# Performance work log

Hardware: AMD Instinct MI355X
Metric: run time of the kernel (lower is better)

Reference implementation:

```python
import jax, jax.numpy as jnp
import numpy as np
import math

DIM = 384
NH = 8
HR = 4.0
LOGIT_MAX = math.log(1.0 / 0.01)
EPS_LN = 1e-5
EPS_NORM = 1e-12


def setup_inputs() -> dict:
    key = jax.random.key(0)
    ks = jax.random.split(key, 6)
    B, C, H, W = 16, DIM, 64, 64
    hid = int(DIM * HR)
    s = lambda k, shape: (jax.random.normal(k, shape, jnp.float32) * 0.02)
    return {
        "x": jax.random.normal(ks[0], (B, C, H, W), jnp.float32),
        "g1": jnp.ones((C,), jnp.float32),
        "beta1": jnp.zeros((C,), jnp.float32),
        "w_qkv": s(ks[1], (3 * C, C)),
        "b_qkv": jnp.zeros((3 * C,), jnp.float32),
        "logit_scale": jnp.log(10.0) * jnp.ones((NH, 1, 1), jnp.float32),
        "w_proj": s(ks[2], (C, C)),
        "b_proj": jnp.zeros((C,), jnp.float32),
        "g2": jnp.ones((C,), jnp.float32),
        "beta2": jnp.zeros((C,), jnp.float32),
        "w_ffn1": s(ks[3], (hid, C)),
        "b_ffn1": jnp.zeros((hid,), jnp.float32),
        "w_ffn2": s(ks[4], (C, hid)),
        "b_ffn2": jnp.zeros((C,), jnp.float32),
    }


def _ln_channels(x, g, b):
    # LayerNorm over channel axis of NCHW (ReshapeLayerNorm equivalent)
    m = x.mean(axis=1, keepdims=True)
    v = x.var(axis=1, keepdims=True)
    return (x - m) / jnp.sqrt(v + EPS_LN) * g[None, :, None, None] + b[None, :, None, None]


def _conv1x1(x, w, b):
    # 1x1 conv == per-pixel matmul: w [O,C], x [B,C,H,W]
    return jnp.einsum('oc,bchw->bohw', w, x) + b[None, :, None, None]


def reference(x, g1, beta1, w_qkv, b_qkv, logit_scale, w_proj, b_proj,
              g2, beta2, w_ffn1, b_ffn1, w_ffn2, b_ffn2):
    B, C, H, W = x.shape
    ch = C // NH  # per-head channel dim

    # --- channel self-attention branch ---
    xn = _ln_channels(x, g1, beta1)
    qkv = _conv1x1(xn, w_qkv, b_qkv)                 # [B, 3C, H, W]
    qkv = qkv.reshape(B, NH, 3 * ch, H * W)          # [B, L, 3c, N]
    q, k, v = jnp.split(qkv, 3, axis=2)              # each [B, L, c, N]

    qn = q / jnp.maximum(jnp.linalg.norm(q, axis=-1, keepdims=True), EPS_NORM)
    kn = k / jnp.maximum(jnp.linalg.norm(k, axis=-1, keepdims=True), EPS_NORM)
    scale = jnp.exp(jnp.minimum(logit_scale, LOGIT_MAX))  # [L,1,1]

    attn = jnp.einsum('blcn,bldn->blcd', qn, kn) * scale[None]  # [B, L, c, c]
    attn = jax.nn.softmax(attn, axis=-1)
    out = jnp.einsum('blcd,bldn->blcn', attn, v)     # [B, L, c, N]
    out = out.reshape(B, C, H, W)
    out = _conv1x1(out, w_proj, b_proj)
    x = x + out

    # --- FFN branch ---
    yn = _ln_channels(x, g2, beta2)
    h = jax.nn.gelu(_conv1x1(yn, w_ffn1, b_ffn1), approximate=False)
    ff = _conv1x1(h, w_ffn2, b_ffn2)
    return x + ff
```

## Files before the change

kernel.cpp:

```cpp
#include <hip/hip_runtime.h>
#include <hip/hip_bf16.h>

#define DIM 384
#define NH 8
#define CH 48
#define NPIX 4096
#define LOGIT_MAX 4.6051701859880914f

typedef unsigned int uint;
typedef __attribute__((ext_vector_type(4))) float f32x4;
typedef __attribute__((ext_vector_type(8))) short bf16x8;

union f2u { float f; uint u; };
__device__ __forceinline__ float bf_lo(uint u) { f2u t; t.u = u << 16; return t.f; }
__device__ __forceinline__ float bf_hi(uint u) { f2u t; t.u = u & 0xffff0000u; return t.f; }
__device__ __forceinline__ unsigned short bfbits(float f) {
  __hip_bfloat16 h = __float2bfloat16(f);
  return *reinterpret_cast<unsigned short*>(&h);
}

__device__ __forceinline__ void gload16(const void* g, void* l) {
  using gp = const __attribute__((address_space(1))) uint*;
  using lp = __attribute__((address_space(3))) uint*;
  __builtin_amdgcn_global_load_lds((gp)(unsigned long long)g,
                                   (lp)(uint)(unsigned long long)l, 16, 0, 0);
}

#define LNP 390
__global__ __launch_bounds__(256) void ln_t_kernel(const float* __restrict__ x,
                                                   const float* __restrict__ g,
                                                   const float* __restrict__ be,
                                                   __hip_bfloat16* __restrict__ out) {
  __shared__ __hip_bfloat16 T[64 * LNP];
  __shared__ float ps1[4][64], ps2[4][64], mArr[64], iArr[64];
  int b = blockIdx.y, n0 = blockIdx.x * 64;
  int nl = threadIdx.x & 63, cg = threadIdx.x >> 6;
  const float* xb = x + ((size_t)b * DIM) * NPIX + n0 + nl;
  float s1 = 0.f, s2 = 0.f;
#pragma unroll 4
  for (int i = 0; i < 96; ++i) {
    int c = cg * 96 + i;
    float v = xb[(size_t)c * NPIX];
    s1 += v; s2 += v * v;
    T[nl * LNP + c] = __float2bfloat16(v);
  }
  ps1[cg][nl] = s1; ps2[cg][nl] = s2;
  __syncthreads();
  if (threadIdx.x < 64) {
    float a = ps1[0][nl] + ps1[1][nl] + ps1[2][nl] + ps1[3][nl];
    float q = ps2[0][nl] + ps2[1][nl] + ps2[2][nl] + ps2[3][nl];
    float m = a * (1.f / DIM);
    float var = q * (1.f / DIM) - m * m;
    mArr[nl] = m;
    iArr[nl] = rsqrtf(var + 1e-5f);
  }
  __syncthreads();
  float m = mArr[nl], inv = iArr[nl];
#pragma unroll 4
  for (int i = 0; i < 96; ++i) {
    int c = cg * 96 + i;
    float v = __bfloat162float(T[nl * LNP + c]);
    v = (v - m) * inv * g[c] + be[c];
    T[nl * LNP + c] = __float2bfloat16(v);
  }
  __syncthreads();
  uint* ob = (uint*)(out + ((size_t)b * NPIX + n0) * DIM);
#pragma unroll 4
  for (int it = 0; it < 48; ++it) {
    int gi = it * 256 + threadIdx.x;
    int n = gi / 192, c2 = gi % 192;
    uint w = *(const uint*)((const char*)T + n * (LNP * 2) + c2 * 4);
    ob[gi] = w;
  }
}

template <int PIX, int GELU_ACT, int RES>
__global__ __launch_bounds__(256) void mfma_gemm(const __hip_bfloat16* __restrict__ Wb,
                                                 const float* __restrict__ bias,
                                                 const __hip_bfloat16* __restrict__ X,
                                                 int XN, int xn0,
                                                 void* __restrict__ outp, int ON, int on0,
                                                 const float* __restrict__ Res, int O, int K) {
  __shared__ alignas(16) __hip_bfloat16 lw[2][4096];
  __shared__ alignas(16) __hip_bfloat16 lx[2][4096];
  const int b = blockIdx.z;
  const int n0 = blockIdx.x * 128, o0 = blockIdx.y * 128;
  const int tid = threadIdx.x, lane = tid & 63, wv = tid >> 6;
  const int srow = lane >> 2;
  const int ksl = ((lane & 3) ^ ((srow >> 1) & 3)) * 8;
  const __hip_bfloat16* srcW = Wb + (size_t)(o0 + wv * 32 + srow) * K + ksl;
  const __hip_bfloat16* srcX = X + ((size_t)b * XN + xn0 + n0 + wv * 32 + srow) * K + ksl;
  f32x4 acc[4][4];
#pragma unroll
  for (int i = 0; i < 4; ++i)
#pragma unroll
    for (int j = 0; j < 4; ++j) acc[i][j] = {0.f, 0.f, 0.f, 0.f};
  const int lrow = lane & 15, ko = lane >> 4;
  const int swz = ko ^ ((lrow >> 1) & 3);
  const int wr0 = (wv >> 1) * 64, wc0 = (wv & 1) * 64;

  auto STAGE = [&](int buf, int k0) {
    __hip_bfloat16* dW = &lw[buf][wv * 1024];
    __hip_bfloat16* dX = &lx[buf][wv * 1024];
    gload16(srcW + k0, dW);
    gload16(srcW + (size_t)16 * K + k0, dW + 512);
    gload16(srcX + k0, dX);
    gload16(srcX + (size_t)16 * K + k0, dX + 512);
  };
  auto COMPUTE = [&](int buf) {
    const bf16x8* lAv = (const bf16x8*)(PIX ? lw[buf] : lx[buf]);
    const bf16x8* lBv = (const bf16x8*)(PIX ? lx[buf] : lw[buf]);
    bf16x8 af[4], bfv[4];
#pragma unroll
    for (int i = 0; i < 4; ++i) af[i] = lAv[(wr0 + i * 16 + lrow) * 4 + swz];
#pragma unroll
    for (int j = 0; j < 4; ++j) bfv[j] = lBv[(wc0 + j * 16 + lrow) * 4 + swz];
#pragma unroll
    for (int i = 0; i < 4; ++i)
#pragma unroll
      for (int j = 0; j < 4; ++j)
        acc[i][j] = __builtin_amdgcn_mfma_f32_16x16x32_bf16(af[i], bfv[j], acc[i][j], 0, 0, 0);
  };

  const int nk = K >> 5;
  STAGE(0, 0);
  STAGE(1, 32);
  for (int t = 0; t < nk; ++t) {
    if (t + 1 < nk) {
      asm volatile("s_waitcnt vmcnt(4)" ::: "memory");
    } else {
      asm volatile("s_waitcnt vmcnt(0)" ::: "memory");
    }
    __builtin_amdgcn_s_barrier();
    COMPUTE(t & 1);
    if (t + 2 < nk) {
      __builtin_amdgcn_s_barrier();
      __builtin_amdgcn_sched_barrier(0);
      STAGE(t & 1, (t + 2) * 32);
    }
  }

  if (PIX) {
    __hip_bfloat16* ob = (__hip_bfloat16*)outp + ((size_t)b * ON + on0) * O;
#pragma unroll
    for (int i = 0; i < 4; ++i) {
      int ob0 = o0 + wr0 + i * 16 + ko * 4;
      float bv[4] = {bias[ob0], bias[ob0 + 1], bias[ob0 + 2], bias[ob0 + 3]};
#pragma unroll
      for (int j = 0; j < 4; ++j) {
        int n = n0 + wc0 + j * 16 + lrow;
        float v[4];
#pragma unroll
        for (int r = 0; r < 4; ++r) {
          v[r] = acc[i][j][r] + bv[r];
          if (GELU_ACT) v[r] = v[r] * 0.5f * (1.f + erff(v[r] * 0.70710678118f));
        }
        *(ushort4*)(ob + (size_t)n * O + ob0) =
            make_ushort4(bfbits(v[0]), bfbits(v[1]), bfbits(v[2]), bfbits(v[3]));
      }
    }
  } else {
    float* of = (float*)outp;
#pragma unroll
    for (int i = 0; i < 4; ++i) {
      int nb0 = on0 + n0 + wr0 + i * 16 + ko * 4;
#pragma unroll
      for (int j = 0; j < 4; ++j) {
        int o = o0 + wc0 + j * 16 + lrow;
        size_t idx = ((size_t)b * O + o) * 4096 + nb0;
        float bv = bias[o];
        float4 w;
        w.x = acc[i][j][0] + bv; w.y = acc[i][j][1] + bv;
        w.z = acc[i][j][2] + bv; w.w = acc[i][j][3] + bv;
        if (RES) {
          const float4 rr = *(const float4*)&Res[idx];
          w.x += rr.x; w.y += rr.y; w.z += rr.z; w.w += rr.w;
        }
        *(float4*)&of[idx] = w;
      }
    }
  }
}

__global__ __launch_bounds__(256) void qk_a(const __hip_bfloat16* __restrict__ qkv,
                                            float* __restrict__ ps,
                                            float* __restrict__ pss)
{
  __shared__ float T[64][100];
  __shared__ float ssq_red[192];
  int bl = blockIdx.y, b = bl >> 3, lh = bl & 7;
  int chunk = blockIdx.x;
  int tid = threadIdx.x;
  int i0 = (tid >> 4) * 3, j0 = (tid & 15) * 3;
  int ch = tid % 96, ph = tid / 96;
  float s[3][3] = {};
  float ssq = 0.f;
  for (int sub = 0; sub < 8; ++sub) {
    int nc = chunk * 512 + sub * 64;
    __syncthreads();
#pragma unroll
    for (int it = 0; it < 3; ++it) {
      int q = it * 256 + tid;
      int row = q / 12, part = q % 12;
      uint4 u = *(const uint4*)(qkv + ((size_t)b * NPIX + nc + row) * 1152 + lh * 144 + part * 8);
      float* tp = &T[row][part * 8];
      tp[0] = bf_lo(u.x); tp[1] = bf_hi(u.x); tp[2] = bf_lo(u.y); tp[3] = bf_hi(u.y);
      tp[4] = bf_lo(u.z); tp[5] = bf_hi(u.z); tp[6] = bf_lo(u.w); tp[7] = bf_hi(u.w);
    }
    __syncthreads();
#pragma unroll 4
    for (int n = 0; n < 64; ++n) {
      float qa0 = T[n][i0], qa1 = T[n][i0 + 1], qa2 = T[n][i0 + 2];
      float kb0 = T[n][48 + j0], kb1 = T[n][48 + j0 + 1], kb2 = T[n][48 + j0 + 2];
      s[0][0] += qa0 * kb0; s[0][1] += qa0 * kb1; s[0][2] += qa0 * kb2;
      s[1][0] += qa1 * kb0; s[1][1] += qa1 * kb1; s[1][2] += qa1 * kb2;
      s[2][0] += qa2 * kb0; s[2][1] += qa2 * kb1; s[2][2] += qa2 * kb2;
    }
    if (ph < 2) {
#pragma unroll 8
      for (int px = ph * 32; px < ph * 32 + 32; ++px) {
        float v = T[px][ch];
        ssq += v * v;
      }
    }
  }
  float* sp = ps + ((size_t)bl * 8 + chunk) * 2304;
#pragma unroll
  for (int a = 0; a < 3; ++a)
#pragma unroll
    for (int bb = 0; bb < 3; ++bb) sp[(i0 + a) * 48 + j0 + bb] = s[a][bb];
  __syncthreads();
  if (ph < 2) ssq_red[ph * 96 + ch] = ssq;
  __syncthreads();
  if (tid < 96) pss[((size_t)bl * 8 + chunk) * 96 + tid] = ssq_red[tid] + ssq_red[96 + tid];
}

__global__ __launch_bounds__(256) void qk_b(const float* __restrict__ ps,
                                            const float* __restrict__ pss,
                                            const float* __restrict__ lsc,
                                            __hip_bfloat16* __restrict__ attn_bf) {
  __shared__ float inv_s[96];
  __shared__ float S[2304];
  int bl = blockIdx.x, lh = bl & 7;
  int tid = threadIdx.x;
  if (tid < 96) {
    float s = 0.f;
#pragma unroll
    for (int c = 0; c < 8; ++c) s += pss[((size_t)bl * 8 + c) * 96 + tid];
    inv_s[tid] = 1.f / fmaxf(sqrtf(s), 1e-12f);
  }
  __syncthreads();
  float scale = expf(fminf(lsc[lh], LOGIT_MAX));
#pragma unroll
  for (int r = 0; r < 9; ++r) {
    int e = r * 256 + tid;
    float s = 0.f;
#pragma unroll
    for (int c = 0; c < 8; ++c) s += ps[((size_t)bl * 8 + c) * 2304 + e];
    int i = e / 48, j = e % 48;
    S[e] = s * inv_s[i] * inv_s[48 + j] * scale;
  }
  __syncthreads();
  if (tid < 48) {
    int i = tid;
    float mx = -1e30f;
    for (int j = 0; j < 48; ++j) mx = fmaxf(mx, S[i * 48 + j]);
    float sum = 0.f;
    for (int j = 0; j < 48; ++j) {
      float ev = expf(S[i * 48 + j] - mx);
      S[i * 48 + j] = ev;
      sum += ev;
    }
    float r = 1.f / sum;
    __hip_bfloat16* ap = attn_bf + (size_t)bl * 3072 + i * 64;
    for (int j = 0; j < 48; ++j) ap[j] = __float2bfloat16(S[i * 48 + j] * r);
    for (int j = 48; j < 64; ++j) ap[j] = __float2bfloat16(0.f);
  }
}

__global__ __launch_bounds__(256) void av_mfma(const __hip_bfloat16* __restrict__ attn_bf,
                                               const __hip_bfloat16* __restrict__ qkv,
                                               __hip_bfloat16* __restrict__ aout,
                                               const __hip_bfloat16* __restrict__ zb) {
  __shared__ alignas(16) __hip_bfloat16 la[3072];
  __shared__ alignas(16) __hip_bfloat16 lv[8192];
  int bl = blockIdx.y, b = bl >> 3, lh = bl & 7;
  int n0 = blockIdx.x * 128;
  int tid = threadIdx.x, lane = tid & 63, wv = tid >> 6;
  {
    int r = lane >> 3, sl = lane & 7;
    for (int c = wv; c < 6; c += 4) {
      int row = c * 8 + r;
      int sp = sl ^ (row & 7);
      gload16(attn_bf + (size_t)bl * 3072 + row * 64 + sp * 8, la + c * 512);
    }
#pragma unroll
    for (int i = 0; i < 4; ++i) {
      int c = wv * 4 + i;
      int row = c * 8 + r;
      int sp = sl ^ (row & 7);
      const __hip_bfloat16* src =
          (sp < 6) ? qkv + ((size_t)b * NPIX + n0 + row) * 1152 + lh * 144 + 96 + sp * 8 : zb;
      gload16(src, lv + c * 512);
    }
  }
  __syncthreads();
  int lrow = lane & 15, ko = lane >> 4;
  f32x4 acc[3][2];
#pragma unroll
  for (int cf = 0; cf < 3; ++cf)
#pragma unroll
    for (int nf = 0; nf < 2; ++nf) acc[cf][nf] = {0.f, 0.f, 0.f, 0.f};
  const bf16x8* lav = (const bf16x8*)la;
  const bf16x8* lvv = (const bf16x8*)lv;
#pragma unroll
  for (int ks = 0; ks < 2; ++ks) {
    bf16x8 a[3], vb[2];
#pragma unroll
    for (int cf = 0; cf < 3; ++cf) {
      int c = cf * 16 + lrow;
      a[cf] = lav[c * 8 + ((ks * 4 + ko) ^ (c & 7))];
    }
#pragma unroll
    for (int nf = 0; nf < 2; ++nf) {
      int n = wv * 32 + nf * 16 + lrow;
      vb[nf] = lvv[n * 8 + ((ks * 4 + ko) ^ (n & 7))];
    }
#pragma unroll
    for (int cf = 0; cf < 3; ++cf)
#pragma unroll
      for (int nf = 0; nf < 2; ++nf)
        acc[cf][nf] = __builtin_amdgcn_mfma_f32_16x16x32_bf16(a[cf], vb[nf], acc[cf][nf], 0, 0, 0);
  }
#pragma unroll
  for (int cf = 0; cf < 3; ++cf)
#pragma unroll
    for (int nf = 0; nf < 2; ++nf) {
      int n = n0 + wv * 32 + nf * 16 + lrow;
      int c = cf * 16 + ko * 4;
      *(ushort4*)(aout + ((size_t)b * NPIX + n) * DIM + lh * CH + c) =
          make_ushort4(bfbits(acc[cf][nf][0]), bfbits(acc[cf][nf][1]),
                       bfbits(acc[cf][nf][2]), bfbits(acc[cf][nf][3]));
    }
}

__global__ __launch_bounds__(256) void wcvt4(const float* __restrict__ w,
                                             __hip_bfloat16* __restrict__ o, int n4) {
  int i = blockIdx.x * 256 + threadIdx.x;
  if (i >= n4) return;
  float4 v = ((const float4*)w)[i];
  ((ushort4*)o)[i] = make_ushort4(bfbits(v.x), bfbits(v.y), bfbits(v.z), bfbits(v.w));
}

extern "C" void kernel_launch(void* const* d_in, const int* in_sizes, int n_in,
                              void* d_out, int out_size, void* d_ws, size_t ws_size,
                              hipStream_t stream) {
  (void)in_sizes; (void)n_in; (void)out_size; (void)ws_size;
  const float* x      = (const float*)d_in[0];
  const float* g1     = (const float*)d_in[1];
  const float* beta1  = (const float*)d_in[2];
  const float* w_qkv  = (const float*)d_in[3];
  const float* b_qkv  = (const float*)d_in[4];
  const float* lsc    = (const float*)d_in[5];
  const float* w_proj = (const float*)d_in[6];
  const float* b_proj = (const float*)d_in[7];
  const float* g2     = (const float*)d_in[8];
  const float* beta2  = (const float*)d_in[9];
  const float* w_ffn1 = (const float*)d_in[10];
  const float* b_ffn1 = (const float*)d_in[11];
  const float* w_ffn2 = (const float*)d_in[12];
  const float* b_ffn2 = (const float*)d_in[13];
  float* out = (float*)d_out;

  char* ws = (char*)d_ws;
  __hip_bfloat16* xn     = (__hip_bfloat16*)(ws);
  __hip_bfloat16* qkv    = (__hip_bfloat16*)(ws + 50331648ull);
  __hip_bfloat16* hbuf   = (__hip_bfloat16*)(ws + 50331648ull);
  __hip_bfloat16* wffn1b = (__hip_bfloat16*)(ws + 151000064ull);
  __hip_bfloat16* wffn2b = (__hip_bfloat16*)(ws + 152179712ull);
  __hip_bfloat16* aout   = (__hip_bfloat16*)(ws + 201326592ull);
  __hip_bfloat16* wqkvb  = (__hip_bfloat16*)(ws + 201326592ull);
  float*          ps     = (float*)(ws + 201326592ull);
  float*          pss    = (float*)(ws + 210763776ull);
  const size_t T0 = 251658240ull;
  __hip_bfloat16* attnb  = (__hip_bfloat16*)(ws + T0 + 49152ull);
  __hip_bfloat16* zb     = (__hip_bfloat16*)(ws + T0 + 835584ull);
  __hip_bfloat16* wprojb = (__hip_bfloat16*)(ws + T0 + 835840ull);

  (void)hipMemsetAsync(zb, 0, 256, stream);
  wcvt4<<<432, 256, 0, stream>>>(w_qkv, wqkvb, 110592);
  wcvt4<<<144, 256, 0, stream>>>(w_proj, wprojb, 36864);

  ln_t_kernel<<<dim3(64, 16), 256, 0, stream>>>(x, g1, beta1, xn);
  mfma_gemm<1, 0, 0><<<dim3(32, 9, 16), 256, 0, stream>>>(wqkvb, b_qkv, xn, 4096, 0,
                                                          qkv, 4096, 0, nullptr, 1152, 384);
  qk_a<<<dim3(8, 128), 256, 0, stream>>>(qkv, ps, pss);
  qk_b<<<128, 256, 0, stream>>>(ps, pss, lsc, attnb);
  av_mfma<<<dim3(32, 128), 256, 0, stream>>>(attnb, qkv, aout, zb);
  mfma_gemm<0, 0, 1><<<dim3(32, 3, 16), 256, 0, stream>>>(wprojb, b_proj, aout, 4096, 0,
                                                          d_out, 4096, 0, x, 384, 384);

  wcvt4<<<576, 256, 0, stream>>>(w_ffn1, wffn1b, 147456);
  wcvt4<<<576, 256, 0, stream>>>(w_ffn2, wffn2b, 147456);
  ln_t_kernel<<<dim3(64, 16), 256, 0, stream>>>(out, g2, beta2, xn);
  for (int h = 0; h < 2; ++h) {
    mfma_gemm<1, 1, 0><<<dim3(16, 12, 16), 256, 0, stream>>>(wffn1b, b_ffn1, xn, 4096, h * 2048,
                                                             hbuf, 2048, 0, nullptr, 1536, 384);
    mfma_gemm<0, 0, 1><<<dim3(16, 3, 16), 256, 0, stream>>>(wffn2b, b_ffn2, hbuf, 2048, 0,
                                                            d_out, 4096, h * 2048, (const float*)out,
                                                            384, 1536);
  }
}
```

Baseline: 785.5 us.

## Triple-buffer GEMM K-loop with one barrier per step and LDS-staged bf16 epilogue

Replaces the double-buffered K loop, which used two barriers per iteration, with a three-buffer rotation. Each step waits, takes one barrier, issues the next stage's global-to-LDS loads, then runs the MFMAs, so loads overlap compute better and barrier count halves. The PIX-path bf16 output is first transposed through LDS and then written with coalesced 16-byte stores instead of scattered 8-byte stores. LDS use rises from 32KB to 48KB per block, which may reduce occupancy. The unrolled loop assumes K/32 is a multiple of three.

Result: faster. 749.1 us (-4.6%).

```diff
diff --git a/kernel.cpp b/kernel.cpp
--- a/kernel.cpp
+++ b/kernel.cpp
@@ -81,8 +81,7 @@
                                                  int XN, int xn0,
                                                  void* __restrict__ outp, int ON, int on0,
                                                  const float* __restrict__ Res, int O, int K) {
-  __shared__ alignas(16) __hip_bfloat16 lw[2][4096];
-  __shared__ alignas(16) __hip_bfloat16 lx[2][4096];
+  __shared__ alignas(16) __hip_bfloat16 smem[3 * 8192];
   const int b = blockIdx.z;
   const int n0 = blockIdx.x * 128, o0 = blockIdx.y * 128;
   const int tid = threadIdx.x, lane = tid & 63, wv = tid >> 6;
@@ -100,16 +99,15 @@
   const int wr0 = (wv >> 1) * 64, wc0 = (wv & 1) * 64;
 
   auto STAGE = [&](int buf, int k0) {
-    __hip_bfloat16* dW = &lw[buf][wv * 1024];
-    __hip_bfloat16* dX = &lx[buf][wv * 1024];
-    gload16(srcW + k0, dW);
-    gload16(srcW + (size_t)16 * K + k0, dW + 512);
-    gload16(srcX + k0, dX);
-    gload16(srcX + (size_t)16 * K + k0, dX + 512);
+    __hip_bfloat16* base = smem + buf * 8192 + wv * 1024;
+    gload16(srcW + k0, base);
+    gload16(srcW + (size_t)16 * K + k0, base + 512);
+    gload16(srcX + k0, base + 4096);
+    gload16(srcX + (size_t)16 * K + k0, base + 4096 + 512);
   };
   auto COMPUTE = [&](int buf) {
-    const bf16x8* lAv = (const bf16x8*)(PIX ? lw[buf] : lx[buf]);
-    const bf16x8* lBv = (const bf16x8*)(PIX ? lx[buf] : lw[buf]);
+    const bf16x8* lAv = (const bf16x8*)(smem + buf * 8192 + (PIX ? 0 : 4096));
+    const bf16x8* lBv = (const bf16x8*)(smem + buf * 8192 + (PIX ? 4096 : 0));
     bf16x8 af[4], bfv[4];
 #pragma unroll
     for (int i = 0; i < 4; ++i) af[i] = lAv[(wr0 + i * 16 + lrow) * 4 + swz];
@@ -121,43 +119,56 @@
       for (int j = 0; j < 4; ++j)
         acc[i][j] = __builtin_amdgcn_mfma_f32_16x16x32_bf16(af[i], bfv[j], acc[i][j], 0, 0, 0);
   };
+  auto FULL = [&](int t, int cb, int sb) {
+    asm volatile("s_waitcnt vmcnt(4)" ::: "memory");
+    __builtin_amdgcn_s_barrier();
+    STAGE(sb, (t + 2) * 32);
+    COMPUTE(cb);
+  };
 
   const int nk = K >> 5;
   STAGE(0, 0);
   STAGE(1, 32);
-  for (int t = 0; t < nk; ++t) {
-    if (t + 1 < nk) {
-      asm volatile("s_waitcnt vmcnt(4)" ::: "memory");
-    } else {
-      asm volatile("s_waitcnt vmcnt(0)" ::: "memory");
-    }
-    __builtin_amdgcn_s_barrier();
-    COMPUTE(t & 1);
-    if (t + 2 < nk) {
-      __builtin_amdgcn_s_barrier();
-      __builtin_amdgcn_sched_barrier(0);
-      STAGE(t & 1, (t + 2) * 32);
-    }
-  }
+  int t = 0;
+  for (; t + 3 < nk; t += 3) {
+    FULL(t, 0, 2); FULL(t + 1, 1, 0); FULL(t + 2, 2, 1);
+  }
+  FULL(nk - 3, 0, 2);
+  asm volatile("s_waitcnt vmcnt(4)" ::: "memory");
+  __builtin_amdgcn_s_barrier();
+  COMPUTE(1);
+  asm volatile("s_waitcnt vmcnt(0)" ::: "memory");
+  __builtin_amdgcn_s_barrier();
+  COMPUTE(2);
 
   if (PIX) {
-    __hip_bfloat16* ob = (__hip_bfloat16*)outp + ((size_t)b * ON + on0) * O;
+    __syncthreads();
 #pragma unroll
     for (int i = 0; i < 4; ++i) {
-      int ob0 = o0 + wr0 + i * 16 + ko * 4;
-      float bv[4] = {bias[ob0], bias[ob0 + 1], bias[ob0 + 2], bias[ob0 + 3]};
+      int o_l = wr0 + i * 16 + ko * 4;
+      int og = o0 + o_l;
+      float bv[4] = {bias[og], bias[og + 1], bias[og + 2], bias[og + 3]};
 #pragma unroll
       for (int j = 0; j < 4; ++j) {
-        int n = n0 + wc0 + j * 16 + lrow;
+        int n_l = wc0 + j * 16 + lrow;
         float v[4];
 #pragma unroll
         for (int r = 0; r < 4; ++r) {
           v[r] = acc[i][j][r] + bv[r];
           if (GELU_ACT) v[r] = v[r] * 0.5f * (1.f + erff(v[r] * 0.70710678118f));
         }
-        *(ushort4*)(ob + (size_t)n * O + ob0) =
+        *(ushort4*)&smem[n_l * 136 + o_l] =
             make_ushort4(bfbits(v[0]), bfbits(v[1]), bfbits(v[2]), bfbits(v[3]));
       }
+    }
+    __syncthreads();
+    __hip_bfloat16* ob = (__hip_bfloat16*)outp + ((size_t)b * ON + on0 + n0) * O + o0;
+#pragma unroll
+    for (int it = 0; it < 8; ++it) {
+      int gi = it * 256 + tid;
+      int n = gi >> 4, c = gi & 15;
+      uint4 wq = *(const uint4*)&smem[n * 136 + c * 8];
+      *(uint4*)(ob + (size_t)n * O + c * 8) = wq;
     }
   } else {
     float* of = (float*)outp;
```
